# Performance work log

Hardware: AMD Instinct MI355X
Metric: run time of the kernel (lower is better)

## Reference

```python
import jax, jax.numpy as jnp
import numpy as np

EMBED_DIM = 384
HEADS = 6
HEAD_DIM = EMBED_DIM // HEADS
WINDOW = 64


def setup_inputs() -> dict:
    key = jax.random.key(0)
    ks = jax.random.split(key, 5)
    B, T = 128, 256
    s_attn = 1.0 / np.sqrt(EMBED_DIM)
    x = jax.random.normal(ks[0], (B, T, EMBED_DIM), dtype=jnp.float32)
    W_attn = jax.random.normal(ks[1], (EMBED_DIM, 3 * EMBED_DIM), dtype=jnp.float32) * s_attn
    b_attn = jax.random.normal(ks[2], (3 * EMBED_DIM,), dtype=jnp.float32) * 0.02
    W_proj = jax.random.normal(ks[3], (EMBED_DIM, EMBED_DIM), dtype=jnp.float32) * s_attn
    b_proj = jax.random.normal(ks[4], (EMBED_DIM,), dtype=jnp.float32) * 0.02
    return {"x": x, "W_attn": W_attn, "b_attn": b_attn, "W_proj": W_proj, "b_proj": b_proj}


def reference(x, W_attn, b_attn, W_proj, b_proj):
    B, T, C = x.shape
    qkv = x @ W_attn + b_attn  # [B,T,3C]
    q, k, v = jnp.split(qkv, 3, axis=-1)
    # [B, H, T, hd]
    q = q.reshape(B, T, HEADS, HEAD_DIM).transpose(0, 2, 1, 3)
    k = k.reshape(B, T, HEADS, HEAD_DIM).transpose(0, 2, 1, 3)
    v = v.reshape(B, T, HEADS, HEAD_DIM).transpose(0, 2, 1, 3)
    scale = 1.0 / np.sqrt(HEAD_DIM).astype(np.float32)
    att = jnp.einsum('bhqd,bhkd->bhqk', q, k) * scale
    i = jnp.arange(T)
    causal = i[:, None] >= i[None, :]
    local = jnp.abs(i[:, None] - i[None, :]) <= WINDOW
    mask = (causal & local)[None, None, :, :]
    att = jnp.where(mask, att, -jnp.inf)
    att = jax.nn.softmax(att, axis=-1)
    y = jnp.einsum('bhqk,bhkd->bhqd', att, v)
    y = y.transpose(0, 2, 1, 3).reshape(B, T, C)
    return y @ W_proj + b_proj
```

## Files before the change

### kernel.cpp

```cpp
#include <hip/hip_runtime.h>

#define B_SZ   128
#define T_SEQ  256
#define C_DIM  384
#define HEADS  6
#define HD     64
#define WIN    64

typedef __bf16 bf16x8 __attribute__((ext_vector_type(8)));
typedef float  f32x4  __attribute__((ext_vector_type(4)));

typedef __attribute__((address_space(3))) void lds_void;
typedef __attribute__((address_space(1))) void gbl_void;

__device__ __forceinline__ unsigned short f2bf(float f) {
  unsigned u = __float_as_uint(f);
  u += 0x7FFFu + ((u >> 16) & 1u);
  return (unsigned short)(u >> 16);
}


__global__ __launch_bounds__(256) void convert_pack_f32_bf16(
    const float* __restrict__ in, unsigned short* __restrict__ out) {
  const int tid = blockIdx.x * 256 + threadIdx.x;
  const int m   = tid / 48;
  const int rem = tid % 48;
  const int kc  = rem >> 2;
  const int u   = rem & 3;
  const float4 a = *(const float4*)(in + (size_t)m * 384 + kc * 32 + u * 8);
  const float4 b = *(const float4*)(in + (size_t)m * 384 + kc * 32 + u * 8 + 4);
  const int p = u ^ ((m & 7) >> 1);
  unsigned short* dst =
      out + ((size_t)(m >> 7) * 12 + kc) * 4096 + (m & 127) * 32 + p * 8;
  ushort4 o1, o2;
  o1.x = f2bf(a.x); o1.y = f2bf(a.y); o1.z = f2bf(a.z); o1.w = f2bf(a.w);
  o2.x = f2bf(b.x); o2.y = f2bf(b.y); o2.z = f2bf(b.z); o2.w = f2bf(b.w);
  *(ushort4*)dst = o1;
  *(ushort4*)(dst + 4) = o2;
}

__global__ __launch_bounds__(256) void transpose_convert_pack(
    const float* __restrict__ in, unsigned short* __restrict__ out,
    int K, int N) {
  __shared__ float tile[32][33];
  const int gx = blockIdx.x * 32;
  const int gy = blockIdx.y * 32;
  const int tx = threadIdx.x;
  const int ty = threadIdx.y;
#pragma unroll
  for (int r = ty; r < 32; r += 8)
    tile[r][tx] = in[(size_t)(gy + r) * N + gx + tx];
  __syncthreads();
  const int nkc = K >> 5;
#pragma unroll
  for (int r = ty; r < 32; r += 8) {
    const int n = gx + r;
    const int k = gy + tx;
    const int p = (((k >> 3) & 3) ^ ((n & 7) >> 1));
    out[((size_t)(n >> 7) * nkc + (k >> 5)) * 4096 + (n & 127) * 32 + p * 8 +
        (k & 7)] = f2bf(tile[tx][r]);
  }
}

template <bool OUT_BF16, int KK>
__global__ __launch_bounds__(256, 3) void gemm_mfma_bf16(
    const unsigned short* __restrict__ A,
    const unsigned short* __restrict__ Bt,
    const float* __restrict__ bias,
    void* __restrict__ Cv, int M, int N, int tiles_n) {
  __shared__ __attribute__((aligned(16))) char smem_raw[49152];
  float* ep = (float*)smem_raw;

  constexpr int NK = KK / 32;

  const int t    = threadIdx.x;
  const int lane = t & 63;
  const int w    = t >> 6;
  const int wr   = w >> 1;
  const int wc   = w & 1;

  const unsigned id    = blockIdx.x;
  const unsigned remap = (id & 7u) * (gridDim.x >> 3) + (id >> 3);
  const int by = remap / (unsigned)tiles_n;
  const int bx = remap % (unsigned)tiles_n;
  const int m0 = by * 128;
  const int n0 = bx * 128;

  const unsigned short* Atile = A  + (size_t)by * NK * 4096;
  const unsigned short* Btile = Bt + (size_t)bx * NK * 4096;

  const int m16  = lane & 15;
  const int quad = lane >> 4;
  const int cp   = (quad ^ ((m16 >> 1) & 3)) << 3;

  f32x4 acc[4][4];
#pragma unroll
  for (int i = 0; i < 4; ++i)
#pragma unroll
    for (int j = 0; j < 4; ++j) acc[i][j] = (f32x4){0.f, 0.f, 0.f, 0.f};

  auto stage = [&](int slot, int kc) {
    unsigned short* Ad = (unsigned short*)(smem_raw + slot * 16384);
    unsigned short* Bd = Ad + 128 * 32;
    const unsigned short* ta = Atile + (size_t)kc * 4096;
    const unsigned short* tb = Btile + (size_t)kc * 4096;
#pragma unroll
    for (int i = 0; i < 2; ++i) {
      const int inst = w * 2 + i;
      __builtin_amdgcn_global_load_lds(
          (const gbl_void*)(ta + inst * 512 + lane * 8),
          (lds_void*)(Ad + inst * 512), 16, 0, 0);
      __builtin_amdgcn_global_load_lds(
          (const gbl_void*)(tb + inst * 512 + lane * 8),
          (lds_void*)(Bd + inst * 512), 16, 0, 0);
    }
  };

  stage(0, 0);
  stage(1, 1);

#pragma unroll
  for (int kt = 0; kt < NK; ++kt) {
    if (kt + 1 < NK)
      asm volatile("s_waitcnt vmcnt(4) lgkmcnt(0)" ::: "memory");
    else
      asm volatile("s_waitcnt vmcnt(0) lgkmcnt(0)" ::: "memory");
    __builtin_amdgcn_s_barrier();
    __builtin_amdgcn_sched_barrier(0);

    if (kt + 2 < NK) stage((kt + 2) % 3, kt + 2);

    const unsigned short* Ac =
        (const unsigned short*)(smem_raw + (kt % 3) * 16384);
    const unsigned short* Bc = Ac + 128 * 32;

    bf16x8 af[4];
#pragma unroll
    for (int mt = 0; mt < 4; ++mt)
      af[mt] = *(const bf16x8*)(Ac + (size_t)(wr * 64 + mt * 16 + m16) * 32 + cp);
#pragma unroll
    for (int nt = 0; nt < 4; ++nt) {
      bf16x8 bfr = *(const bf16x8*)(Bc + (size_t)(wc * 64 + nt * 16 + m16) * 32 + cp);
#pragma unroll
      for (int mt = 0; mt < 4; ++mt)
        acc[mt][nt] = __builtin_amdgcn_mfma_f32_16x16x32_bf16(
            af[mt], bfr, acc[mt][nt], 0, 0, 0);
    }
  }
  __syncthreads();

  float bv[4];
#pragma unroll
  for (int nt = 0; nt < 4; ++nt) bv[nt] = bias[n0 + wc * 64 + nt * 16 + m16];

#pragma unroll
  for (int p = 0; p < 2; ++p) {
    if (p) __syncthreads();
    if (wr == p) {
#pragma unroll
      for (int mt = 0; mt < 4; ++mt)
#pragma unroll
        for (int nt = 0; nt < 4; ++nt)
#pragma unroll
          for (int r = 0; r < 4; ++r)
            ep[(mt * 16 + quad * 4 + r) * 132 + wc * 64 + nt * 16 + m16] =
                acc[mt][nt][r] + bv[nt];
    }
    __syncthreads();
#pragma unroll
    for (int cc = 0; cc < 8; ++cc) {
      const int chunk = cc * 256 + t;
      const int row = chunk >> 5;
      const int c4  = chunk & 31;
      f32x4 v = *(const f32x4*)(ep + row * 132 + c4 * 4);
      const int grow = m0 + p * 64 + row;
      const int gcol = n0 + c4 * 4;
      if (OUT_BF16) {
        ushort4 o;
        o.x = f2bf(v[0]); o.y = f2bf(v[1]); o.z = f2bf(v[2]); o.w = f2bf(v[3]);
        *(ushort4*)((unsigned short*)Cv + (size_t)grow * N + gcol) = o;
      } else {
        *(f32x4*)((float*)Cv + (size_t)grow * N + gcol) = v;
      }
    }
  }
}

#define PSTR 68
__global__ __launch_bounds__(256) void attn_mfma(
    const unsigned short* __restrict__ qkv, unsigned short* __restrict__ y) {
  __shared__ unsigned short Qs[64 * 64];
  __shared__ unsigned short Ks[64 * 64];
  __shared__ unsigned short Vt[64 * 64];
  __shared__ float Pw[4][16 * PSTR];

  const unsigned id  = blockIdx.x;
  const unsigned bid = (id & 7u) * (gridDim.x >> 3) + (id >> 3);
  const int qt  = bid & 3;
  const int h   = (bid >> 2) % HEADS;
  const int b   = bid / (4 * HEADS);
  const int t   = threadIdx.x;
  const int lane = t & 63;
  const int w    = t >> 6;
  const int quad = lane >> 4;
  const int m16  = lane & 15;
  const int sw   = m16 & 7;

  const size_t rowbase = (size_t)b * T_SEQ * (3 * C_DIM);
  const int qoff = h * HD;
  const int koff = C_DIM + h * HD;
  const int voff = 2 * C_DIM + h * HD;
  const int qg0  = qt * 64;

  const int lrow = lane >> 3;
  const int lcol = lane & 7;
  const int schunk = lcol ^ lrow;

#pragma unroll
  for (int i = 0; i < 2; ++i) {
    const int inst = w * 2 + i;
    const int r = inst * 8 + lrow;
    const unsigned short* ga =
        qkv + rowbase + (size_t)(qg0 + r) * (3 * C_DIM) + qoff + schunk * 8;
    __builtin_amdgcn_global_load_lds((const gbl_void*)ga,
                                     (lds_void*)(Qs + inst * 512), 16, 0, 0);
  }

  float m_r[4], l_r[4];
  f32x4 yacc[4];
#pragma unroll
  for (int r = 0; r < 4; ++r) { m_r[r] = -1e30f; l_r[r] = 0.f; }
#pragma unroll
  for (int dt = 0; dt < 4; ++dt) yacc[dt] = (f32x4){0.f, 0.f, 0.f, 0.f};

  const int nchunks  = (qt == 0) ? 1 : 2;
  const int kb_first = (qt == 0) ? 0 : (qg0 - 64);
  const int qrow_base = qg0 + w * 16 + quad * 4;

  for (int ch = 0; ch < nchunks; ++ch) {
    const int kb = kb_first + ch * 64;

    __syncthreads();

#pragma unroll
    for (int i = 0; i < 2; ++i) {
      const int inst = w * 2 + i;
      const int r = inst * 8 + lrow;
      const unsigned short* ga =
          qkv + rowbase + (size_t)(kb + r) * (3 * C_DIM) + koff + schunk * 8;
      __builtin_amdgcn_global_load_lds((const gbl_void*)ga,
                                       (lds_void*)(Ks + inst * 512), 16, 0, 0);
    }
    {
      const int vkey = t & 63;
      const int kc = vkey >> 3, ke = vkey & 7;
      const int vd0  = (t >> 6) * 16;
      const unsigned short* gv =
          qkv + rowbase + (size_t)(kb + vkey) * (3 * C_DIM) + voff + vd0;
#pragma unroll
      for (int u = 0; u < 4; ++u) {
        ushort4 vv = *(const ushort4*)(gv + u * 4);
#pragma unroll
        for (int jj = 0; jj < 4; ++jj) {
          const int d = vd0 + u * 4 + jj;
          const unsigned short val =
              (jj == 0) ? vv.x : (jj == 1) ? vv.y : (jj == 2) ? vv.z : vv.w;
          Vt[d * 64 + ((kc ^ (d & 7)) << 3) + ke] = val;
        }
      }
    }
    __syncthreads();

    f32x4 sacc[4];
#pragma unroll
    for (int nt = 0; nt < 4; ++nt) sacc[nt] = (f32x4){0.f, 0.f, 0.f, 0.f};
#pragma unroll
    for (int ks = 0; ks < 64; ks += 32) {
      const int cp = (((ks >> 3) + quad) ^ sw) << 3;
      bf16x8 aq = *(const bf16x8*)(Qs + (size_t)(w * 16 + m16) * 64 + cp);
#pragma unroll
      for (int nt = 0; nt < 4; ++nt) {
        bf16x8 kf = *(const bf16x8*)(Ks + (size_t)(nt * 16 + m16) * 64 + cp);
        sacc[nt] = __builtin_amdgcn_mfma_f32_16x16x32_bf16(aq, kf, sacc[nt], 0, 0, 0);
      }
    }

    float mc[4] = {-1e30f, -1e30f, -1e30f, -1e30f};
#pragma unroll
    for (int nt = 0; nt < 4; ++nt) {
      const int kg = kb + nt * 16 + m16;
#pragma unroll
      for (int r = 0; r < 4; ++r) {
        const int qg = qrow_base + r;
        const bool valid = (kg <= qg) && (qg - kg <= WIN);
        const float sv = valid ? (sacc[nt][r] * 0.125f) : -1e30f;
        sacc[nt][r] = sv;
        mc[r] = fmaxf(mc[r], sv);
      }
    }
#pragma unroll
    for (int r = 0; r < 4; ++r) {
#pragma unroll
      for (int x = 1; x <= 8; x <<= 1) mc[r] = fmaxf(mc[r], __shfl_xor(mc[r], x));
    }

#pragma unroll
    for (int r = 0; r < 4; ++r) {
      const float mn    = fmaxf(m_r[r], mc[r]);
      const float alpha = __expf(m_r[r] - mn);
      m_r[r] = mn;
      l_r[r] *= alpha;
#pragma unroll
      for (int dt = 0; dt < 4; ++dt) yacc[dt][r] *= alpha;
      float ls = 0.f;
#pragma unroll
      for (int nt = 0; nt < 4; ++nt) {
        const float p = __expf(sacc[nt][r] - mn);
        sacc[nt][r] = p;
        ls += p;
      }
#pragma unroll
      for (int x = 1; x <= 8; x <<= 1) ls += __shfl_xor(ls, x);
      l_r[r] += ls;
    }

#pragma unroll
    for (int nt = 0; nt < 4; ++nt)
#pragma unroll
      for (int r = 0; r < 4; ++r)
        Pw[w][(quad * 4 + r) * PSTR + nt * 16 + m16] = sacc[nt][r];

#pragma unroll
    for (int ks = 0; ks < 64; ks += 32) {
      f32x4 pa = *(const f32x4*)(&Pw[w][m16 * PSTR + ks + quad * 8]);
      f32x4 pb = *(const f32x4*)(&Pw[w][m16 * PSTR + ks + quad * 8 + 4]);
      bf16x8 ap;
#pragma unroll
      for (int j = 0; j < 4; ++j) {
        ap[j]     = (__bf16)pa[j];
        ap[4 + j] = (__bf16)pb[j];
      }
      const int cp = (((ks >> 3) + quad) ^ sw) << 3;
#pragma unroll
      for (int dt = 0; dt < 4; ++dt) {
        bf16x8 vf = *(const bf16x8*)(Vt + (size_t)(dt * 16 + m16) * 64 + cp);
        yacc[dt] = __builtin_amdgcn_mfma_f32_16x16x32_bf16(ap, vf, yacc[dt], 0, 0, 0);
      }
    }
  }

  float* epy = &Pw[0][0];
  float inv[4];
#pragma unroll
  for (int r = 0; r < 4; ++r) inv[r] = 1.f / l_r[r];
#pragma unroll
  for (int dt = 0; dt < 4; ++dt)
#pragma unroll
    for (int r = 0; r < 4; ++r)
      epy[(w * 16 + quad * 4 + r) * PSTR + dt * 16 + m16] = yacc[dt][r] * inv[r];
  __syncthreads();
#pragma unroll
  for (int cc = 0; cc < 4; ++cc) {
    const int chunk = cc * 256 + t;
    const int row = chunk >> 4;
    const int c4  = chunk & 15;
    f32x4 v = *(const f32x4*)(epy + row * PSTR + c4 * 4);
    ushort4 o;
    o.x = f2bf(v[0]); o.y = f2bf(v[1]); o.z = f2bf(v[2]); o.w = f2bf(v[3]);
    const int m = b * T_SEQ + qg0 + row;
    const int c = h * HD + c4 * 4;
    const int kc = c >> 5;
    const int u  = (c >> 3) & 3;
    const int p  = u ^ ((m & 7) >> 1);
    *(ushort4*)(y + ((size_t)(m >> 7) * 12 + kc) * 4096 + (m & 127) * 32 +
                p * 8 + (c & 7)) = o;
  }
}

extern "C" void kernel_launch(void* const* d_in, const int* in_sizes, int n_in,
                              void* d_out, int out_size, void* d_ws, size_t ws_size,
                              hipStream_t stream) {
  const float* x      = (const float*)d_in[0];
  const float* W_attn = (const float*)d_in[1];
  const float* b_attn = (const float*)d_in[2];
  const float* W_proj = (const float*)d_in[3];
  const float* b_proj = (const float*)d_in[4];
  float* out = (float*)d_out;

  const int M = B_SZ * T_SEQ;

  unsigned short* qkv_b = (unsigned short*)d_ws;
  unsigned short* y_b   = qkv_b + (size_t)M * (3 * C_DIM);
  unsigned short* x_b   = y_b   + (size_t)M * C_DIM;
  unsigned short* Wa_t  = x_b   + (size_t)M * C_DIM;
  unsigned short* Wp_t  = Wa_t  + (size_t)(3 * C_DIM) * C_DIM;

  {
    convert_pack_f32_bf16<<<dim3(M * 48 / 256), 256, 0, stream>>>(x, x_b);
    transpose_convert_pack<<<dim3((3 * C_DIM) / 32, C_DIM / 32), dim3(32, 8), 0,
                             stream>>>(W_attn, Wa_t, C_DIM, 3 * C_DIM);
    transpose_convert_pack<<<dim3(C_DIM / 32, C_DIM / 32), dim3(32, 8), 0,
                             stream>>>(W_proj, Wp_t, C_DIM, C_DIM);
  }

  gemm_mfma_bf16<true, C_DIM><<<dim3(9 * (M / 128)), 256, 0, stream>>>(
      x_b, Wa_t, b_attn, qkv_b, M, 3 * C_DIM, 9);

  attn_mfma<<<dim3(B_SZ * HEADS * (T_SEQ / 64)), 256, 0, stream>>>(qkv_b, y_b);

  gemm_mfma_bf16<false, C_DIM><<<dim3(3 * (M / 128)), 256, 0, stream>>>(
      y_b, Wp_t, b_proj, out, M, C_DIM, 3);
}
```

Measured before the change: 191.5 us.

## Write QKV GEMM output in head-major pre-swizzled panes for attention loads

The QKV projection epilogue now scatters its bf16 output into per-(batch, q/k/v, head) contiguous [T, 64] panes, with Q and K pre-XOR-swizzled to match the attention kernel's LDS layout. The attention kernel then loads Q and K tiles as fully contiguous 8 KB blocks with global_load_lds, and reads V from a compact pane, instead of strided rows of the packed [T, 3C] buffer. This is meant to improve coalescing and remove per-lane swizzle address math on the attention side. In exchange, the GEMM stores become 8-byte scattered writes across panes, which may be less efficient.

After: 189.7 us. Within noise of the previous version (-1.0%).

```diff
diff --git a/kernel.cpp b/kernel.cpp
--- a/kernel.cpp
+++ b/kernel.cpp
@@ -153,6 +153,9 @@
 #pragma unroll
   for (int nt = 0; nt < 4; ++nt) bv[nt] = bias[n0 + wc * 64 + nt * 16 + m16];
 
+  const int which = bx / 3;
+  const int hbase = (bx % 3) * 2;
+
 #pragma unroll
   for (int p = 0; p < 2; ++p) {
     if (p) __syncthreads();
@@ -174,12 +177,21 @@
       const int c4  = chunk & 31;
       f32x4 v = *(const f32x4*)(ep + row * 132 + c4 * 4);
       const int grow = m0 + p * 64 + row;
-      const int gcol = n0 + c4 * 4;
       if (OUT_BF16) {
         ushort4 o;
         o.x = f2bf(v[0]); o.y = f2bf(v[1]); o.z = f2bf(v[2]); o.w = f2bf(v[3]);
-        *(ushort4*)((unsigned short*)Cv + (size_t)grow * N + gcol) = o;
+        const int b_ = grow >> 8;
+        const int tp = grow & 255;
+        const int h  = hbase + (c4 >> 4);
+        const int d  = (c4 << 2) & 63;
+        const int dp = (which == 2)
+                           ? d
+                           : ((((d >> 3) ^ (tp & 7)) << 3) | (d & 7));
+        *(ushort4*)((unsigned short*)Cv +
+                    ((size_t)((b_ * 3 + which) * HEADS + h) * T_SEQ + tp) * HD +
+                    dp) = o;
       } else {
+        const int gcol = n0 + c4 * 4;
         *(f32x4*)((float*)Cv + (size_t)grow * N + gcol) = v;
       }
     }
@@ -206,24 +218,20 @@
   const int m16  = lane & 15;
   const int sw   = m16 & 7;
 
-  const size_t rowbase = (size_t)b * T_SEQ * (3 * C_DIM);
-  const int qoff = h * HD;
-  const int koff = C_DIM + h * HD;
-  const int voff = 2 * C_DIM + h * HD;
-  const int qg0  = qt * 64;
-
-  const int lrow = lane >> 3;
-  const int lcol = lane & 7;
-  const int schunk = lcol ^ lrow;
+  const unsigned short* Qpane =
+      qkv + ((size_t)((b * 3 + 0) * HEADS + h) * T_SEQ) * HD;
+  const unsigned short* Kpane =
+      qkv + ((size_t)((b * 3 + 1) * HEADS + h) * T_SEQ) * HD;
+  const unsigned short* Vpane =
+      qkv + ((size_t)((b * 3 + 2) * HEADS + h) * T_SEQ) * HD;
+  const int qg0 = qt * 64;
 
 #pragma unroll
   for (int i = 0; i < 2; ++i) {
     const int inst = w * 2 + i;
-    const int r = inst * 8 + lrow;
-    const unsigned short* ga =
-        qkv + rowbase + (size_t)(qg0 + r) * (3 * C_DIM) + qoff + schunk * 8;
-    __builtin_amdgcn_global_load_lds((const gbl_void*)ga,
-                                     (lds_void*)(Qs + inst * 512), 16, 0, 0);
+    __builtin_amdgcn_global_load_lds(
+        (const gbl_void*)(Qpane + (size_t)qg0 * HD + inst * 512 + lane * 8),
+        (lds_void*)(Qs + inst * 512), 16, 0, 0);
   }
 
   float m_r[4], l_r[4];
@@ -245,18 +253,15 @@
 #pragma unroll
     for (int i = 0; i < 2; ++i) {
       const int inst = w * 2 + i;
-      const int r = inst * 8 + lrow;
-      const unsigned short* ga =
-          qkv + rowbase + (size_t)(kb + r) * (3 * C_DIM) + koff + schunk * 8;
-      __builtin_amdgcn_global_load_lds((const gbl_void*)ga,
-                                       (lds_void*)(Ks + inst * 512), 16, 0, 0);
+      __builtin_amdgcn_global_load_lds(
+          (const gbl_void*)(Kpane + (size_t)kb * HD + inst * 512 + lane * 8),
+          (lds_void*)(Ks + inst * 512), 16, 0, 0);
     }
     {
       const int vkey = t & 63;
       const int kc = vkey >> 3, ke = vkey & 7;
       const int vd0  = (t >> 6) * 16;
-      const unsigned short* gv =
-          qkv + rowbase + (size_t)(kb + vkey) * (3 * C_DIM) + voff + vd0;
+      const unsigned short* gv = Vpane + (size_t)(kb + vkey) * HD + vd0;
 #pragma unroll
       for (int u = 0; u < 4; ++u) {
         ushort4 vv = *(const ushort4*)(gv + u * 4);
```
